# Optimization experiments

Hardware: AMD Instinct MI355X
Metric: run time of the kernel (lower is better)

Reference implementation:

```python
import jax, jax.numpy as jnp
import numpy as np

D_MODEL = 1024
NUM_HEADS = 16
HEAD_DIM = D_MODEL // NUM_HEADS
B, S = 4, 2048


def setup_inputs() -> dict:
    key = jax.random.key(0)
    ks = jax.random.split(key, 6)
    scale = 1.0 / np.sqrt(D_MODEL)
    return {
        "q": jax.random.normal(ks[0], (B, S, D_MODEL), dtype=jnp.float32),
        "k": jax.random.normal(ks[1], (B, S, D_MODEL), dtype=jnp.float32),
        "v": jax.random.normal(ks[2], (B, S, D_MODEL), dtype=jnp.float32),
        "Wq": jax.random.normal(ks[3], (D_MODEL, D_MODEL), dtype=jnp.float32) * scale,
        "Wk": jax.random.normal(ks[4], (D_MODEL, D_MODEL), dtype=jnp.float32) * scale,
        "Wv": jax.random.normal(ks[5], (D_MODEL, D_MODEL), dtype=jnp.float32) * scale,
    }


def reference(q, k, v, Wq, Wk, Wv):
    b, s, d = q.shape
    # nn.Linear(bias=False): x @ W.T
    qp = jnp.einsum('bsd,ed->bse', q, Wq)
    kp = jnp.einsum('bsd,ed->bse', k, Wk)
    vp = jnp.einsum('bsd,ed->bse', v, Wv)
    # split heads -> (B, H, S, Dh)
    qh = qp.reshape(b, s, NUM_HEADS, HEAD_DIM).transpose(0, 2, 1, 3)
    kh = kp.reshape(b, s, NUM_HEADS, HEAD_DIM).transpose(0, 2, 1, 3)
    vh = vp.reshape(b, s, NUM_HEADS, HEAD_DIM).transpose(0, 2, 1, 3)
    scores = jnp.einsum('bhqd,bhkd->bhqk', qh, kh) / jnp.sqrt(jnp.float32(HEAD_DIM))
    attn = jax.nn.softmax(scores, axis=-1)
    att = jnp.einsum('bhqk,bhkd->bhqd', attn, vh)
    # NOTE: faithful to the source, which does a raw .view (no head transpose back)
    return att.reshape(b, s, d)
```

## Files before the change

### kernel.cpp

```cpp
#include <hip/hip_runtime.h>
#include <hip/hip_bf16.h>
#include <stdint.h>

#define D_MODEL 1024
#define NHEAD   16
#define HDIM    64
#define BATCH   4
#define SEQ     2048
#define NTOK    (BATCH*SEQ)

typedef __bf16          b16x8 __attribute__((ext_vector_type(8)));
typedef unsigned short  u16x8 __attribute__((ext_vector_type(8)));
typedef unsigned short  u16x4 __attribute__((ext_vector_type(4)));
typedef float           f32x4 __attribute__((ext_vector_type(4)));

__device__ __forceinline__ unsigned short f2b(float f) {
  union { float f; uint32_t u; } c; c.f = f;
  return (unsigned short)((c.u + 0x7FFFu + ((c.u >> 16) & 1u)) >> 16);
}

__device__ __forceinline__ uint32_t cvtpk(float lo, float hi) {
  uint32_t r;
  asm("v_cvt_pk_bf16_f32 %0, %1, %2" : "=v"(r) : "v"(lo), "v"(hi));
  return r;
}

__device__ __forceinline__ u16x4 pk4(f32x4 x) {
  union { uint32_t u[2]; u16x4 v; } r;
  r.u[0] = cvtpk(x[0], x[1]);
  r.u[1] = cvtpk(x[2], x[3]);
  return r.v;
}

__device__ __forceinline__ u16x8 pk8(f32x4 a, f32x4 b) {
  union { uint32_t u[4]; u16x8 v; } r;
  r.u[0] = cvtpk(a[0], a[1]);
  r.u[1] = cvtpk(a[2], a[3]);
  r.u[2] = cvtpk(b[0], b[1]);
  r.u[3] = cvtpk(b[2], b[3]);
  return r.v;
}

__device__ __forceinline__ void glds16(const void* g, void* l) {
  __builtin_amdgcn_global_load_lds(
      (const __attribute__((address_space(1))) unsigned int*)g,
      (__attribute__((address_space(3))) unsigned int*)l, 16, 0, 0);
}

__global__ __launch_bounds__(256, 8)
void wpack_kernel(const float* __restrict__ Wq, const float* __restrict__ Wk,
                  const float* __restrict__ Wv, unsigned short* __restrict__ wsp) {
  int bid = blockIdx.x;
  int which = bid >> 8;
  int tn = (bid >> 5) & 7;
  int kt = bid & 31;
  const float* W = (which == 0) ? Wq : ((which == 1) ? Wk : Wv);
  int t = threadIdx.x;
  int r = t >> 1;
  int sw0 = (t & 1) * 2;
  char* dst = (char*)wsp + (size_t)bid * 8192 + t * 32;
  const float* src = W + (size_t)(tn * 128 + r) * D_MODEL + kt * 32;
#pragma unroll
  for (int i = 0; i < 2; i++) {
    int s = (sw0 + i) ^ ((r >> 1) & 3);
    f32x4 a = *(const f32x4*)(src + s * 8);
    f32x4 b = *(const f32x4*)(src + s * 8 + 4);
    *(u16x8*)(dst + i * 16) = pk8(a, b);
  }
}

__global__ __launch_bounds__(256, 5)
void proj_gemm_kernel(const float* __restrict__ q, const float* __restrict__ k,
                      const float* __restrict__ v, const unsigned short* __restrict__ wsp,
                      unsigned short* __restrict__ qp, unsigned short* __restrict__ kp,
                      unsigned short* __restrict__ vt) {
  __shared__ __align__(16) char lds[2][16384];

  int bid = blockIdx.x;
  int swz = (bid & 7) * 192 + (bid >> 3);
  int which = swz >> 9;
  int rr = swz & 511;
  int tm = rr >> 3, tn = rr & 7;

  const float* X = (which == 0) ? q : ((which == 1) ? k : v);
  const char* Bsrc = (const char*)wsp + (size_t)((which * 8 + tn) * 32) * 8192;

  int tid  = threadIdx.x;
  int lane = tid & 63;
  int w    = tid >> 6;
  int g    = lane >> 4;
  int c    = lane & 15;
  int wr   = (w >> 1) * 64;
  int wc   = (w & 1) * 64;

  f32x4 acc[4][4];
#pragma unroll
  for (int m = 0; m < 4; m++)
#pragma unroll
    for (int n = 0; n < 4; n++) acc[m][n] = (f32x4){0.f, 0.f, 0.f, 0.f};

  int srow = tid >> 2, sseg = tid & 3;
  const float* Ag = X + (size_t)(tm * 128 + srow) * D_MODEL + sseg * 8;
  int wbyteA = srow * 64 + ((sseg ^ ((srow >> 1) & 3)) << 4);

  int rco   = ((g ^ ((c >> 1) & 3)) << 4);
  int raoff = (wr + c) * 64 + rco;
  int rboff = 8192 + (wc + c) * 64 + rco;

  int bglane = w * 2048 + lane * 16;

  f32x4 ra0 = *(const f32x4*)(Ag);
  f32x4 ra1 = *(const f32x4*)(Ag + 4);
  f32x4 ra2 = *(const f32x4*)(Ag + 64 * D_MODEL);
  f32x4 ra3 = *(const f32x4*)(Ag + 64 * D_MODEL + 4);
  glds16(Bsrc + bglane,        lds[0] + 8192 + w * 2048);
  glds16(Bsrc + bglane + 1024, lds[0] + 8192 + w * 2048 + 1024);
  *(u16x8*)(lds[0] + wbyteA)        = pk8(ra0, ra1);
  *(u16x8*)(lds[0] + wbyteA + 4096) = pk8(ra2, ra3);

  for (int kt = 0; kt < 32; kt++) {
    __syncthreads();
    char* nb = lds[(kt + 1) & 1];
    if (kt < 31) {
      ra0 = *(const f32x4*)(Ag + (kt + 1) * 32);
      ra1 = *(const f32x4*)(Ag + (kt + 1) * 32 + 4);
      ra2 = *(const f32x4*)(Ag + 64 * D_MODEL + (kt + 1) * 32);
      ra3 = *(const f32x4*)(Ag + 64 * D_MODEL + (kt + 1) * 32 + 4);
      glds16(Bsrc + (size_t)(kt + 1) * 8192 + bglane,        nb + 8192 + w * 2048);
      glds16(Bsrc + (size_t)(kt + 1) * 8192 + bglane + 1024, nb + 8192 + w * 2048 + 1024);
    }
    const char* buf = lds[kt & 1];
    u16x8 af[4], bf[4];
#pragma unroll
    for (int m = 0; m < 4; m++)
      af[m] = *(const u16x8*)(buf + raoff + m * 1024);
#pragma unroll
    for (int n = 0; n < 4; n++)
      bf[n] = *(const u16x8*)(buf + rboff + n * 1024);
#pragma unroll
    for (int m = 0; m < 4; m++)
#pragma unroll
      for (int n = 0; n < 4; n++)
        acc[m][n] = __builtin_amdgcn_mfma_f32_16x16x32_bf16(
            __builtin_bit_cast(b16x8, af[m]), __builtin_bit_cast(b16x8, bf[n]),
            acc[m][n], 0, 0, 0);
    if (kt < 31) {
      *(u16x8*)(nb + wbyteA)        = pk8(ra0, ra1);
      *(u16x8*)(nb + wbyteA + 4096) = pk8(ra2, ra3);
    }
  }

  int cbase = tn * 128 + wc;
  int rbase = tm * 128 + wr;
  if (which < 2) {
    unsigned short* OutP = (which == 0) ? qp : kp;
    float scale = (which == 0) ? 0.18033688f : 1.0f;
#pragma unroll
    for (int m = 0; m < 4; m++)
#pragma unroll
      for (int n = 0; n < 4; n++) {
        int e = cbase + n * 16 + c;
        int h = e >> 6, dh = e & 63;
#pragma unroll
        for (int j = 0; j < 4; j++) {
          int i = rbase + m * 16 + g * 4 + j;
          int b = i >> 11, s = i & 2047;
          OutP[(((size_t)(b * NHEAD + h)) * SEQ + s) * HDIM + dh] =
              f2b(acc[m][n][j] * scale);
        }
      }
  } else {
#pragma unroll
    for (int m = 0; m < 4; m++)
#pragma unroll
      for (int n = 0; n < 4; n++) {
        int e = cbase + n * 16 + c;
        int h = e >> 6, dh = e & 63;
        int i0 = rbase + m * 16 + g * 4;
        int b = i0 >> 11, s0 = i0 & 2047;
        *(u16x4*)&vt[(((size_t)(b * NHEAD + h)) * HDIM + dh) * SEQ + s0] = pk4(acc[m][n]);
      }
  }
}

#define KVB 64
__global__ __launch_bounds__(256, 3)
void attn_kernel(const unsigned short* __restrict__ qp,
                 const unsigned short* __restrict__ kp,
                 const unsigned short* __restrict__ vt,
                 float* __restrict__ out) {
  __shared__ __align__(16) char lds[2][16384];

  int bid = blockIdx.x;
  int swz = (bid & 7) * 128 + (bid >> 3);
  int bh = swz >> 4;
  int qb = swz & 15;

  int tid  = threadIdx.x;
  int lane = tid & 63;
  int w    = tid >> 6;
  int g    = lane >> 4;
  int c    = lane & 15;
  int chi  = c & 7;

  const unsigned short* Kg = kp + (size_t)bh * SEQ * HDIM;
  const unsigned short* Vg = vt + (size_t)bh * HDIM * SEQ;

  int q0 = qb * 128 + w * 32;
  u16x8 qf[2][2];
#pragma unroll
  for (int qg = 0; qg < 2; qg++)
#pragma unroll
    for (int h = 0; h < 2; h++)
      qf[qg][h] = *(const u16x8*)&qp[((size_t)bh * SEQ + q0 + qg * 16 + c) * HDIM + h * 32 + g * 8];

  f32x4 o[4][2];
#pragma unroll
  for (int d = 0; d < 4; d++)
#pragma unroll
    for (int qg = 0; qg < 2; qg++) o[d][qg] = (f32x4){0.f, 0.f, 0.f, 0.f};
  float l[2] = {0.f, 0.f};

  int koffA = c * 128 + ((g * 16) ^ (chi << 4));
  int koffB = c * 128 + (((64 + g * 16)) ^ (chi << 4));
  int voff[2][2];
#pragma unroll
  for (int w2 = 0; w2 < 2; w2++) {
    int b0 = w2 * 64 + g * 8;
    voff[w2][0] = 8192 + c * 128 + ((((b0      >> 4) ^ chi) << 4) + (b0 & 15));
    voff[w2][1] = 8192 + c * 128 + (((((b0+32) >> 4) ^ chi) << 4) + (b0 & 15));
  }
  int arow = tid >> 3, aseg = tid & 7;
  int kwo = arow * 128 + ((aseg * 16) ^ ((arow & 7) << 4));
  int vwo = 8192 + kwo;

  char* cur = lds[0];
  char* nxt = lds[1];

  u16x8 kreg[2], vreg[2];
  kreg[0] = *(const u16x8*)&Kg[(size_t)arow * HDIM + aseg * 8];
  kreg[1] = *(const u16x8*)&Kg[(size_t)(arow + 32) * HDIM + aseg * 8];
  vreg[0] = *(const u16x8*)&Vg[(size_t)arow * SEQ + aseg * 8];
  vreg[1] = *(const u16x8*)&Vg[(size_t)(arow + 32) * SEQ + aseg * 8];
  *(u16x8*)(cur + kwo)        = kreg[0];
  *(u16x8*)(cur + kwo + 4096) = kreg[1];
  *(u16x8*)(cur + vwo)        = vreg[0];
  *(u16x8*)(cur + vwo + 4096) = vreg[1];
  __syncthreads();

  for (int t = 0; t < SEQ / KVB; t++) {
    if (t < SEQ / KVB - 1) {
      int kv1 = (t + 1) * KVB;
      kreg[0] = *(const u16x8*)&Kg[(size_t)(kv1 + arow) * HDIM + aseg * 8];
      kreg[1] = *(const u16x8*)&Kg[(size_t)(kv1 + arow + 32) * HDIM + aseg * 8];
      vreg[0] = *(const u16x8*)&Vg[(size_t)arow * SEQ + kv1 + aseg * 8];
      vreg[1] = *(const u16x8*)&Vg[(size_t)(arow + 32) * SEQ + kv1 + aseg * 8];
    }

    f32x4 sf[4][2];
#pragma unroll
    for (int st = 0; st < 4; st++) {
      u16x8 kf0 = *(const u16x8*)(cur + koffA + st * 2048);
      u16x8 kf1 = *(const u16x8*)(cur + koffB + st * 2048);
#pragma unroll
      for (int qg = 0; qg < 2; qg++) {
        sf[st][qg] = __builtin_amdgcn_mfma_f32_16x16x32_bf16(
            __builtin_bit_cast(b16x8, kf0), __builtin_bit_cast(b16x8, qf[qg][0]),
            (f32x4){0.f, 0.f, 0.f, 0.f}, 0, 0, 0);
        sf[st][qg] = __builtin_amdgcn_mfma_f32_16x16x32_bf16(
            __builtin_bit_cast(b16x8, kf1), __builtin_bit_cast(b16x8, qf[qg][1]),
            sf[st][qg], 0, 0, 0);
      }
    }

    union { uint32_t u[4]; u16x8 v; } pb[2][2];
#pragma unroll
    for (int qg = 0; qg < 2; qg++) {
      float p[4][4];
#pragma unroll
      for (int st = 0; st < 4; st++)
#pragma unroll
        for (int j = 0; j < 4; j++) p[st][j] = exp2f(sf[st][qg][j]);
      float s01 = ((p[0][0] + p[0][1]) + (p[0][2] + p[0][3])) +
                  ((p[1][0] + p[1][1]) + (p[1][2] + p[1][3]));
      float s23 = ((p[2][0] + p[2][1]) + (p[2][2] + p[2][3])) +
                  ((p[3][0] + p[3][1]) + (p[3][2] + p[3][3]));
      l[qg] += s01 + s23;
#pragma unroll
      for (int w2 = 0; w2 < 2; w2++) {
        pb[w2][qg].u[0] = cvtpk(p[2*w2][0],   p[2*w2][1]);
        pb[w2][qg].u[1] = cvtpk(p[2*w2][2],   p[2*w2][3]);
        pb[w2][qg].u[2] = cvtpk(p[2*w2+1][0], p[2*w2+1][1]);
        pb[w2][qg].u[3] = cvtpk(p[2*w2+1][2], p[2*w2+1][3]);
      }
    }

#pragma unroll
    for (int w2 = 0; w2 < 2; w2++)
#pragma unroll
      for (int d = 0; d < 4; d++) {
        union { u16x4 h[2]; u16x8 v; } afu;
        afu.h[0] = *(const u16x4*)(cur + voff[w2][0] + d * 2048);
        afu.h[1] = *(const u16x4*)(cur + voff[w2][1] + d * 2048);
#pragma unroll
        for (int qg = 0; qg < 2; qg++)
          o[d][qg] = __builtin_amdgcn_mfma_f32_16x16x32_bf16(
              __builtin_bit_cast(b16x8, afu.v), __builtin_bit_cast(b16x8, pb[w2][qg].v),
              o[d][qg], 0, 0, 0);
      }

    if (t < SEQ / KVB - 1) {
      *(u16x8*)(nxt + kwo)        = kreg[0];
      *(u16x8*)(nxt + kwo + 4096) = kreg[1];
      *(u16x8*)(nxt + vwo)        = vreg[0];
      *(u16x8*)(nxt + vwo + 4096) = vreg[1];
    }
    __syncthreads();
    char* tmp = cur; cur = nxt; nxt = tmp;
  }

#pragma unroll
  for (int qg = 0; qg < 2; qg++) {
    l[qg] += __shfl_xor(l[qg], 16);
    l[qg] += __shfl_xor(l[qg], 32);
  }
#pragma unroll
  for (int qg = 0; qg < 2; qg++) {
    float inv = 1.f / l[qg];
    float* orow = out + ((size_t)bh * SEQ + q0 + qg * 16 + c) * HDIM;
#pragma unroll
    for (int d = 0; d < 4; d++) {
      f32x4 val;
#pragma unroll
      for (int j = 0; j < 4; j++) val[j] = o[d][qg][j] * inv;
      *(f32x4*)(orow + d * 16 + g * 4) = val;
    }
  }
}

extern "C" void kernel_launch(void* const* d_in, const int* in_sizes, int n_in,
                              void* d_out, int out_size, void* d_ws, size_t ws_size,
                              hipStream_t stream) {
  const float* q  = (const float*)d_in[0];
  const float* k  = (const float*)d_in[1];
  const float* v  = (const float*)d_in[2];
  const float* Wq = (const float*)d_in[3];
  const float* Wk = (const float*)d_in[4];
  const float* Wv = (const float*)d_in[5];

  unsigned short* qp  = (unsigned short*)d_ws;
  unsigned short* kp  = qp + (size_t)NTOK * D_MODEL;
  unsigned short* vt  = kp + (size_t)NTOK * D_MODEL;
  unsigned short* wsp = vt + (size_t)NTOK * D_MODEL;
  float* out = (float*)d_out;

  hipLaunchKernelGGL(wpack_kernel, dim3(768), dim3(256), 0, stream,
                     Wq, Wk, Wv, wsp);
  hipLaunchKernelGGL(proj_gemm_kernel, dim3(1536), dim3(256), 0, stream,
                     q, k, v, wsp, qp, kp, vt);
  hipLaunchKernelGGL(attn_kernel, dim3(1024), dim3(256), 0, stream,
                     qp, kp, vt, out);
}
```

Before: 200.4 us.

## Stage fp32 activations directly into LDS and convert to bf16 at fragment load

```diff
diff --git a/kernel.cpp b/kernel.cpp
--- a/kernel.cpp
+++ b/kernel.cpp
@@ -25,20 +25,11 @@
   return r;
 }
 
-__device__ __forceinline__ u16x4 pk4(f32x4 x) {
-  union { uint32_t u[2]; u16x4 v; } r;
-  r.u[0] = cvtpk(x[0], x[1]);
-  r.u[1] = cvtpk(x[2], x[3]);
-  return r.v;
-}
-
-__device__ __forceinline__ u16x8 pk8(f32x4 a, f32x4 b) {
-  union { uint32_t u[4]; u16x8 v; } r;
-  r.u[0] = cvtpk(a[0], a[1]);
-  r.u[1] = cvtpk(a[2], a[3]);
-  r.u[2] = cvtpk(b[0], b[1]);
-  r.u[3] = cvtpk(b[2], b[3]);
-  return r.v;
+__device__ __forceinline__ b16x8 cv8(f32x4 a, f32x4 b) {
+  b16x8 r;
+#pragma unroll
+  for (int i = 0; i < 4; i++) { r[i] = (__bf16)a[i]; r[i + 4] = (__bf16)b[i]; }
+  return r;
 }
 
 __device__ __forceinline__ void glds16(const void* g, void* l) {
@@ -65,16 +56,19 @@
     int s = (sw0 + i) ^ ((r >> 1) & 3);
     f32x4 a = *(const f32x4*)(src + s * 8);
     f32x4 b = *(const f32x4*)(src + s * 8 + 4);
-    *(u16x8*)(dst + i * 16) = pk8(a, b);
-  }
-}
-
-__global__ __launch_bounds__(256, 5)
+    u16x8 pk;
+#pragma unroll
+    for (int j = 0; j < 4; j++) { pk[j] = f2b(a[j]); pk[j + 4] = f2b(b[j]); }
+    *(u16x8*)(dst + i * 16) = pk;
+  }
+}
+
+__global__ __launch_bounds__(256, 3)
 void proj_gemm_kernel(const float* __restrict__ q, const float* __restrict__ k,
                       const float* __restrict__ v, const unsigned short* __restrict__ wsp,
                       unsigned short* __restrict__ qp, unsigned short* __restrict__ kp,
                       unsigned short* __restrict__ vt) {
-  __shared__ __align__(16) char lds[2][16384];
+  __shared__ __align__(16) char lds[2][24576];
 
   int bid = blockIdx.x;
   int swz = (bid & 7) * 192 + (bid >> 3);
@@ -83,13 +77,14 @@
   int tm = rr >> 3, tn = rr & 7;
 
   const float* X = (which == 0) ? q : ((which == 1) ? k : v);
-  const char* Bsrc = (const char*)wsp + (size_t)((which * 8 + tn) * 32) * 8192;
+  const char* Bpack = (const char*)wsp + (size_t)((which * 8 + tn) * 32) * 8192;
 
   int tid  = threadIdx.x;
   int lane = tid & 63;
   int w    = tid >> 6;
   int g    = lane >> 4;
   int c    = lane & 15;
+  int chi  = c & 7;
   int wr   = (w >> 1) * 64;
   int wc   = (w & 1) * 64;
 
@@ -99,41 +94,40 @@
 #pragma unroll
     for (int n = 0; n < 4; n++) acc[m][n] = (f32x4){0.f, 0.f, 0.f, 0.f};
 
-  int srow = tid >> 2, sseg = tid & 3;
-  const float* Ag = X + (size_t)(tm * 128 + srow) * D_MODEL + sseg * 8;
-  int wbyteA = srow * 64 + ((sseg ^ ((srow >> 1) & 3)) << 4);
-
-  int rco   = ((g ^ ((c >> 1) & 3)) << 4);
-  int raoff = (wr + c) * 64 + rco;
-  int rboff = 8192 + (wc + c) * 64 + rco;
-
-  int bglane = w * 2048 + lane * 16;
-
-  f32x4 ra0 = *(const f32x4*)(Ag);
-  f32x4 ra1 = *(const f32x4*)(Ag + 4);
-  f32x4 ra2 = *(const f32x4*)(Ag + 64 * D_MODEL);
-  f32x4 ra3 = *(const f32x4*)(Ag + 64 * D_MODEL + 4);
-  glds16(Bsrc + bglane,        lds[0] + 8192 + w * 2048);
-  glds16(Bsrc + bglane + 1024, lds[0] + 8192 + w * 2048 + 1024);
-  *(u16x8*)(lds[0] + wbyteA)        = pk8(ra0, ra1);
-  *(u16x8*)(lds[0] + wbyteA + 4096) = pk8(ra2, ra3);
+  int arowl = lane >> 3;
+  int aswz  = ((lane & 7) ^ arowl) << 4;
+  const char* Asrc = (const char*)(X + (size_t)(tm * 128 + w * 32 + arowl) * D_MODEL) + aswz;
+  const char* Bsrc = Bpack + w * 2048 + lane * 16;
+
+  int aoff0 = (wr + c) * 128 + ((2 * g    ^ chi) << 4);
+  int aoff1 = (wr + c) * 128 + (((2*g+1) ^ chi) << 4);
+  int rboff = 16384 + (wc + c) * 64 + ((g ^ ((c >> 1) & 3)) << 4);
+
+#pragma unroll
+  for (int i = 0; i < 4; i++)
+    glds16(Asrc + (size_t)i * 8 * D_MODEL * 4, lds[0] + w * 4096 + i * 1024);
+  glds16(Bsrc,        lds[0] + 16384 + w * 2048);
+  glds16(Bsrc + 1024, lds[0] + 16384 + w * 2048 + 1024);
 
   for (int kt = 0; kt < 32; kt++) {
     __syncthreads();
-    char* nb = lds[(kt + 1) & 1];
     if (kt < 31) {
-      ra0 = *(const f32x4*)(Ag + (kt + 1) * 32);
-      ra1 = *(const f32x4*)(Ag + (kt + 1) * 32 + 4);
-      ra2 = *(const f32x4*)(Ag + 64 * D_MODEL + (kt + 1) * 32);
-      ra3 = *(const f32x4*)(Ag + 64 * D_MODEL + (kt + 1) * 32 + 4);
-      glds16(Bsrc + (size_t)(kt + 1) * 8192 + bglane,        nb + 8192 + w * 2048);
-      glds16(Bsrc + (size_t)(kt + 1) * 8192 + bglane + 1024, nb + 8192 + w * 2048 + 1024);
+      char* nb = lds[(kt + 1) & 1];
+#pragma unroll
+      for (int i = 0; i < 4; i++)
+        glds16(Asrc + (size_t)i * 8 * D_MODEL * 4 + (kt + 1) * 128, nb + w * 4096 + i * 1024);
+      glds16(Bsrc + (size_t)(kt + 1) * 8192,        nb + 16384 + w * 2048);
+      glds16(Bsrc + (size_t)(kt + 1) * 8192 + 1024, nb + 16384 + w * 2048 + 1024);
     }
     const char* buf = lds[kt & 1];
-    u16x8 af[4], bf[4];
-#pragma unroll
-    for (int m = 0; m < 4; m++)
-      af[m] = *(const u16x8*)(buf + raoff + m * 1024);
+    b16x8 af[4];
+    u16x8 bf[4];
+#pragma unroll
+    for (int m = 0; m < 4; m++) {
+      f32x4 a0 = *(const f32x4*)(buf + aoff0 + m * 2048);
+      f32x4 a1 = *(const f32x4*)(buf + aoff1 + m * 2048);
+      af[m] = cv8(a0, a1);
+    }
 #pragma unroll
     for (int n = 0; n < 4; n++)
       bf[n] = *(const u16x8*)(buf + rboff + n * 1024);
@@ -142,12 +136,7 @@
 #pragma unroll
       for (int n = 0; n < 4; n++)
         acc[m][n] = __builtin_amdgcn_mfma_f32_16x16x32_bf16(
-            __builtin_bit_cast(b16x8, af[m]), __builtin_bit_cast(b16x8, bf[n]),
-            acc[m][n], 0, 0, 0);
-    if (kt < 31) {
-      *(u16x8*)(nb + wbyteA)        = pk8(ra0, ra1);
-      *(u16x8*)(nb + wbyteA + 4096) = pk8(ra2, ra3);
-    }
+            af[m], __builtin_bit_cast(b16x8, bf[n]), acc[m][n], 0, 0, 0);
   }
 
   int cbase = tn * 128 + wc;
@@ -178,7 +167,10 @@
         int h = e >> 6, dh = e & 63;
         int i0 = rbase + m * 16 + g * 4;
         int b = i0 >> 11, s0 = i0 & 2047;
-        *(u16x4*)&vt[(((size_t)(b * NHEAD + h)) * HDIM + dh) * SEQ + s0] = pk4(acc[m][n]);
+        u16x4 pk;
+#pragma unroll
+        for (int j = 0; j < 4; j++) pk[j] = f2b(acc[m][n][j]);
+        *(u16x4*)&vt[(((size_t)(b * NHEAD + h)) * HDIM + dh) * SEQ + s0] = pk;
       }
   }
 }
```

After: 180.1 us. 1.11x faster.
